# Performance work log

Measured on AMD Instinct MI355X. Metric: run time of the kernel, lower is better.

Reference implementation:

```python
import jax, jax.numpy as jnp
import numpy as np

TAU = 0.5

def _projection(z, W1, b1, W2, b2):
    h = jax.nn.elu(z @ W1.T + b1)
    return h @ W2.T + b2

def _normalize(x, eps=1e-12):
    n = jnp.linalg.norm(x, axis=1, keepdims=True)
    return x / jnp.maximum(n, eps)

def setup_inputs() -> dict:
    key = jax.random.key(0)
    k = jax.random.split(key, 6)
    N, D, P = 8192, 256, 256
    s = 1.0 / np.sqrt(D)
    return {
        "z1": jax.random.normal(k[0], (N, D), jnp.float32),
        "z2": jax.random.normal(k[1], (N, D), jnp.float32),
        "W1": jax.random.normal(k[2], (P, D), jnp.float32) * s,
        "b1": jnp.zeros((P,), jnp.float32),
        "W2": jax.random.normal(k[3], (D, P), jnp.float32) * s,
        "b2": jnp.zeros((D,), jnp.float32),
    }

def reference(z1, z2, W1, b1, W2, b2):
    h1 = _projection(z1, W1, b1, W2, b2)
    h2 = _projection(z2, W1, b1, W2, b2)
    n1 = _normalize(h1)
    n2 = _normalize(h2)
    f11 = jnp.exp((n1 @ n1.T) / TAU)  # [N,N]
    f22 = jnp.exp((n2 @ n2.T) / TAU)
    f12 = jnp.exp((n1 @ n2.T) / TAU)
    d12 = jnp.diagonal(f12)
    l1 = -jnp.log(d12 / (f11.sum(1) + f12.sum(1) - jnp.diagonal(f11)))
    # sim(h2,h1) = f12.T: diag same, row-sum = column-sum of f12
    l2 = -jnp.log(d12 / (f22.sum(1) + f12.sum(0) - jnp.diagonal(f22)))
    return (l1 + l2) * 0.5
```

## Files before the change

kernel.cpp:

```cpp
#include <hip/hip_runtime.h>
#include <hip/hip_bf16.h>
#include <hip/hip_fp8.h>
#include <stdint.h>

#define Nn 8192
#define TWO_N 16384
#define INV_TAU 2.0f

typedef unsigned short u16;
typedef unsigned char u8;
typedef __bf16 bf16x8 __attribute__((ext_vector_type(8)));
typedef float f32x4 __attribute__((ext_vector_type(4)));
typedef int i32x8 __attribute__((ext_vector_type(8)));

typedef const __attribute__((address_space(1))) void* gas_ptr;
typedef __attribute__((address_space(3))) void* las_ptr;

__device__ __forceinline__ void async_copy16(const void* g, void* l) {
  __builtin_amdgcn_global_load_lds((gas_ptr)g, (las_ptr)l, 16, 0, 0);
}

__device__ __forceinline__ u16 f2bf(float x) {
  uint32_t u = __float_as_uint(x);
  u = u + 0x7fffu + ((u >> 16) & 1u);
  return (u16)(u >> 16);
}

__global__ __launch_bounds__(256)
void mfma_gemm1(const float* __restrict__ z1, const float* __restrict__ z2,
                const float* __restrict__ W1, const float* __restrict__ bias,
                u16* __restrict__ outp) {
  __shared__ __bf16 sA[128 * 64];
  __shared__ __bf16 sB[128 * 64];
  const int bx = blockIdx.x;
  const int i0 = bx * 128;
  const int j0 = blockIdx.y * 128;
  const float* Zsrc = (bx < 64) ? (z1 + (size_t)i0 * 256) : (z2 + (size_t)(i0 - Nn) * 256);
  const float* Wsrc = W1 + (size_t)j0 * 256;
  const int t = threadIdx.x;
  const int lane = t & 63, wave = t >> 6;
  const int wm = (wave >> 1) * 64, wn = (wave & 1) * 64;
  const int fr = lane >> 4, fc = lane & 15;
  const int sw = fc & 7;

  f32x4 acc[4][4];
#pragma unroll
  for (int a = 0; a < 4; a++)
#pragma unroll
    for (int b = 0; b < 4; b++) acc[a][b] = (f32x4){0.f, 0.f, 0.f, 0.f};

  for (int k0 = 0; k0 < 256; k0 += 64) {
    __syncthreads();
#pragma unroll
    for (int it = 0; it < 4; ++it) {
      int c = t + 256 * it;
      int row = c >> 3;
      int g = (c & 7) ^ (row & 7);
      const float* sa = Zsrc + (size_t)row * 256 + k0 + g * 8;
      float4 a0 = *(const float4*)sa;
      float4 a1 = *(const float4*)(sa + 4);
      bf16x8 va = {(__bf16)a0.x, (__bf16)a0.y, (__bf16)a0.z, (__bf16)a0.w,
                   (__bf16)a1.x, (__bf16)a1.y, (__bf16)a1.z, (__bf16)a1.w};
      *(bf16x8*)&sA[c * 8] = va;
      const float* sb = Wsrc + (size_t)row * 256 + k0 + g * 8;
      float4 b0 = *(const float4*)sb;
      float4 b1v = *(const float4*)(sb + 4);
      bf16x8 vb = {(__bf16)b0.x, (__bf16)b0.y, (__bf16)b0.z, (__bf16)b0.w,
                   (__bf16)b1v.x, (__bf16)b1v.y, (__bf16)b1v.z, (__bf16)b1v.w};
      *(bf16x8*)&sB[c * 8] = vb;
    }
    __syncthreads();
#pragma unroll
    for (int ks = 0; ks < 2; ++ks) {
      bf16x8 af[4], bfr[4];
#pragma unroll
      for (int mi = 0; mi < 4; mi++)
        af[mi] = *(const bf16x8*)&sA[(wm + mi * 16 + fc) * 64 + (((ks * 4 + fr) ^ sw) * 8)];
#pragma unroll
      for (int ni = 0; ni < 4; ni++)
        bfr[ni] = *(const bf16x8*)&sB[(wn + ni * 16 + fc) * 64 + (((ks * 4 + fr) ^ sw) * 8)];
#pragma unroll
      for (int mi = 0; mi < 4; mi++)
#pragma unroll
        for (int ni = 0; ni < 4; ni++)
          acc[mi][ni] = __builtin_amdgcn_mfma_f32_16x16x32_bf16(af[mi], bfr[ni], acc[mi][ni], 0, 0, 0);
    }
  }

#pragma unroll
  for (int mi = 0; mi < 4; mi++) {
#pragma unroll
    for (int ni = 0; ni < 4; ni++) {
      int col = j0 + wn + ni * 16 + fc;
      float bv = bias[col];
#pragma unroll
      for (int r = 0; r < 4; r++) {
        int row = i0 + wm + mi * 16 + fr * 4 + r;
        float v = acc[mi][ni][r] + bv;
        v = v > 0.f ? v : (__expf(v) - 1.f);
        outp[(size_t)row * 256 + col] = f2bf(v);
      }
    }
  }
}

__global__ __launch_bounds__(256)
void gemm2_norm(const u16* __restrict__ A, const float* __restrict__ W2,
                const float* __restrict__ bias, u8* __restrict__ Mf8,
                float* __restrict__ snorm, float* __restrict__ rsum) {
  __shared__ __bf16 sA[128 * 64];
  __shared__ __bf16 sB[256 * 64];
  const int i0 = blockIdx.x * 128;
  const int t = threadIdx.x;
  const int lane = t & 63, wave = t >> 6;
  const int wm = (wave >> 1) * 64, wn = (wave & 1) * 128;
  const int fr = lane >> 4, fc = lane & 15;
  const int sw = fc & 7;

  if (t < 128) rsum[i0 + t] = 0.f;

  f32x4 acc[4][8];
#pragma unroll
  for (int a = 0; a < 4; a++)
#pragma unroll
    for (int b = 0; b < 8; b++) acc[a][b] = (f32x4){0.f, 0.f, 0.f, 0.f};

  const u16* Ag = A + (size_t)i0 * 256;

  for (int k0 = 0; k0 < 256; k0 += 64) {
    __syncthreads();
#pragma unroll
    for (int it = 0; it < 4; ++it) {
      int c = t + 256 * it;
      int row = c >> 3;
      int kc = ((c & 7) ^ (row & 7)) * 8;
      async_copy16(Ag + (size_t)row * 256 + k0 + kc, (void*)&sA[c * 8]);
    }
#pragma unroll
    for (int it = 0; it < 8; ++it) {
      int c = t + 256 * it;
      int row = c >> 3;
      int g = (c & 7) ^ (row & 7);
      const float* sb = W2 + (size_t)row * 256 + k0 + g * 8;
      float4 b0 = *(const float4*)sb;
      float4 b1v = *(const float4*)(sb + 4);
      bf16x8 vb = {(__bf16)b0.x, (__bf16)b0.y, (__bf16)b0.z, (__bf16)b0.w,
                   (__bf16)b1v.x, (__bf16)b1v.y, (__bf16)b1v.z, (__bf16)b1v.w};
      *(bf16x8*)&sB[c * 8] = vb;
    }
    __syncthreads();
#pragma unroll
    for (int ks = 0; ks < 2; ++ks) {
      bf16x8 af[4], bfr[8];
#pragma unroll
      for (int mi = 0; mi < 4; mi++)
        af[mi] = *(const bf16x8*)&sA[(wm + mi * 16 + fc) * 64 + (((ks * 4 + fr) ^ sw) * 8)];
#pragma unroll
      for (int ni = 0; ni < 8; ni++)
        bfr[ni] = *(const bf16x8*)&sB[(wn + ni * 16 + fc) * 64 + (((ks * 4 + fr) ^ sw) * 8)];
#pragma unroll
      for (int mi = 0; mi < 4; mi++)
#pragma unroll
        for (int ni = 0; ni < 8; ni++)
          acc[mi][ni] = __builtin_amdgcn_mfma_f32_16x16x32_bf16(af[mi], bfr[ni], acc[mi][ni], 0, 0, 0);
    }
  }

  float bv[8];
#pragma unroll
  for (int ni = 0; ni < 8; ni++) bv[ni] = bias[wn + ni * 16 + fc];

  __syncthreads();
  float* red = (float*)sA;

#pragma unroll
  for (int mi = 0; mi < 4; mi++) {
    float ssq[4] = {0.f, 0.f, 0.f, 0.f};
#pragma unroll
    for (int ni = 0; ni < 8; ni++)
#pragma unroll
      for (int r = 0; r < 4; r++) {
        float v = acc[mi][ni][r] + bv[ni];
        acc[mi][ni][r] = v;
        ssq[r] += v * v;
      }
#pragma unroll
    for (int r = 0; r < 4; r++) {
      float v = ssq[r];
#pragma unroll
      for (int off = 1; off < 16; off <<= 1) v += __shfl_xor(v, off, 16);
      if (fc == 0) red[(wm + mi * 16 + fr * 4 + r) * 2 + (wn >> 7)] = v;
    }
  }
  __syncthreads();

  float* red2 = red + 256;
#pragma unroll
  for (int mi = 0; mi < 4; mi++) {
    float ssq2[4] = {0.f, 0.f, 0.f, 0.f};
#pragma unroll
    for (int r = 0; r < 4; r++) {
      int row = wm + mi * 16 + fr * 4 + r;
      float ss = red[row * 2] + red[row * 2 + 1];
      float rn = 1.f / fmaxf(sqrtf(ss), 1e-12f);
#pragma unroll
      for (int ni = 0; ni < 8; ni++) {
        float v = acc[mi][ni][r] * rn;
        __hip_fp8_e4m3 q(v);
        Mf8[(size_t)(i0 + row) * 256 + wn + ni * 16 + fc] = q.__x;
        float fv = (float)q;
        ssq2[r] += fv * fv;
      }
    }
#pragma unroll
    for (int r = 0; r < 4; r++) {
      float v = ssq2[r];
#pragma unroll
      for (int off = 1; off < 16; off <<= 1) v += __shfl_xor(v, off, 16);
      if (fc == 0) red2[(wm + mi * 16 + fr * 4 + r) * 2 + (wn >> 7)] = v;
    }
  }
  __syncthreads();
  if (t < 128) snorm[i0 + t] = red2[t * 2] + red2[t * 2 + 1];
}

__global__ __launch_bounds__(256, 2)
void gram_sym(const u8* __restrict__ Mf8, float* __restrict__ rsum) {
  __shared__ u8 sB8[2][128 * 256];
  const int t = threadIdx.x;
  const int lane = t & 63, wave = t >> 6;
  const int wm = (wave >> 1) * 64, wn = (wave & 1) * 64;
  const int fr = lane >> 4, fc = lane & 15;

  int f = 2111 - blockIdx.x;
  int b = 0;
  while (f >= 2 * (b + 1) * (b + 2)) ++b;
  int rem = f - 2 * b * (b + 1);
  int r = rem / (b + 1);
  int q = rem - r * (b + 1);
  int k = 4 * b + 1 + r;
  const int i_t = 128 - k;
  const int jt0 = i_t + 4 * q;
  const int L = min(4, k - 4 * q);
  const int i0 = i_t * 128;

  {
    const u8* Bg = Mf8 + (size_t)jt0 * 128 * 256;
#pragma unroll
    for (int it = 0; it < 8; ++it) {
      int c = t + 256 * it;
      int row = c >> 4, slot = c & 15;
      int g = slot ^ (row & 15);
      async_copy16(Bg + (size_t)row * 256 + g * 16, (void*)&sB8[0][c * 16]);
    }
  }

  i32x8 afr[4][2];
  {
    const u8* Ag = Mf8 + (size_t)i0 * 256;
#pragma unroll
    for (int mi = 0; mi < 4; ++mi) {
      const u8* rp = Ag + (size_t)(wm + mi * 16 + fc) * 256 + fr * 32;
#pragma unroll
      for (int kb = 0; kb < 2; ++kb) {
        int4 lo = *(const int4*)(rp + kb * 128);
        int4 hi = *(const int4*)(rp + kb * 128 + 16);
        afr[mi][kb] = (i32x8){lo.x, lo.y, lo.z, lo.w, hi.x, hi.y, hi.z, hi.w};
      }
    }
  }

  float rowacc[4][4];
#pragma unroll
  for (int a = 0; a < 4; a++)
#pragma unroll
    for (int rr = 0; rr < 4; rr++) rowacc[a][rr] = 0.f;

  for (int jt = 0; jt < L; ++jt) {
    const int j_t = jt0 + jt;
    const int j0 = j_t * 128;
    const u8* sB = &sB8[jt & 1][0];

    __syncthreads();

    if (jt + 1 < L) {
      const u8* Bg = Mf8 + (size_t)(j_t + 1) * 128 * 256;
      u8* dst = &sB8[(jt + 1) & 1][0];
#pragma unroll
      for (int it = 0; it < 8; ++it) {
        int c = t + 256 * it;
        int row = c >> 4, slot = c & 15;
        int g = slot ^ (row & 15);
        async_copy16(Bg + (size_t)row * 256 + g * 16, (void*)&dst[c * 16]);
      }
    }

    f32x4 acc[4][4];
#pragma unroll
    for (int a = 0; a < 4; a++)
#pragma unroll
      for (int bb = 0; bb < 4; bb++) acc[a][bb] = (f32x4){0.f, 0.f, 0.f, 0.f};

#pragma unroll
    for (int kb = 0; kb < 2; ++kb) {
      i32x8 bfrag[4];
#pragma unroll
      for (int ni = 0; ni < 4; ++ni) {
        const u8* base = sB + (wn + ni * 16 + fc) * 256;
        int g0 = kb * 8 + fr * 2;
        int4 lo = *(const int4*)(base + ((g0 ^ fc) * 16));
        int4 hi = *(const int4*)(base + (((g0 + 1) ^ fc) * 16));
        bfrag[ni] = (i32x8){lo.x, lo.y, lo.z, lo.w, hi.x, hi.y, hi.z, hi.w};
      }
#pragma unroll
      for (int mi = 0; mi < 4; mi++)
#pragma unroll
        for (int ni = 0; ni < 4; ni++)
          acc[mi][ni] = __builtin_amdgcn_mfma_scale_f32_16x16x128_f8f6f4(
              afr[mi][kb], bfrag[ni], acc[mi][ni], 0, 0, 0, 0x7F, 0, 0x7F);
    }

    float colp[4] = {0.f, 0.f, 0.f, 0.f};
#pragma unroll
    for (int mi = 0; mi < 4; mi++) {
#pragma unroll
      for (int ni = 0; ni < 4; ni++) {
        float e0 = __expf(acc[mi][ni][0] * INV_TAU);
        float e1 = __expf(acc[mi][ni][1] * INV_TAU);
        float e2 = __expf(acc[mi][ni][2] * INV_TAU);
        float e3 = __expf(acc[mi][ni][3] * INV_TAU);
        rowacc[mi][0] += e0; rowacc[mi][1] += e1;
        rowacc[mi][2] += e2; rowacc[mi][3] += e3;
        colp[ni] += e0 + e1 + e2 + e3;
      }
    }
    if (j_t != i_t) {
#pragma unroll
      for (int ni = 0; ni < 4; ni++) {
        float v = colp[ni];
        v += __shfl_xor(v, 16, 64);
        v += __shfl_xor(v, 32, 64);
        if (fr == 0) atomicAdd(&rsum[j0 + wn + ni * 16 + fc], v);
      }
    }
  }

#pragma unroll
  for (int mi = 0; mi < 4; mi++) {
#pragma unroll
    for (int rr = 0; rr < 4; rr++) {
      float v = rowacc[mi][rr];
#pragma unroll
      for (int off = 1; off < 16; off <<= 1) v += __shfl_xor(v, off, 16);
      rowacc[mi][rr] = v;
    }
  }
  if (fc == 0) {
#pragma unroll
    for (int mi = 0; mi < 4; mi++) {
      int rbase = i0 + wm + mi * 16 + fr * 4;
      atomicAdd(&rsum[rbase + 0], rowacc[mi][0]);
      atomicAdd(&rsum[rbase + 1], rowacc[mi][1]);
      atomicAdd(&rsum[rbase + 2], rowacc[mi][2]);
      atomicAdd(&rsum[rbase + 3], rowacc[mi][3]);
    }
  }
}

__global__ void final_loss(const u8* __restrict__ Mf8, const float* __restrict__ rsum,
                           const float* __restrict__ snorm, float* __restrict__ out) {
  int i = blockIdx.x * 4 + (threadIdx.x >> 6);
  int lane = threadIdx.x & 63;
  unsigned int ua = ((const unsigned int*)(Mf8 + (size_t)i * 256))[lane];
  unsigned int ub = ((const unsigned int*)(Mf8 + (size_t)(Nn + i) * 256))[lane];
  float d = 0.f;
#pragma unroll
  for (int e = 0; e < 4; ++e) {
    __hip_fp8_e4m3 qa, qb;
    qa.__x = (ua >> (8 * e)) & 0xFF;
    qb.__x = (ub >> (8 * e)) & 0xFF;
    d += (float)qa * (float)qb;
  }
#pragma unroll
  for (int off = 32; off; off >>= 1) d += __shfl_xor(d, off, 64);
  if (lane == 0) {
    float den1 = rsum[i] - __expf(snorm[i] * INV_TAU);
    float den2 = rsum[Nn + i] - __expf(snorm[Nn + i] * INV_TAU);
    out[i] = 0.5f * (logf(den1) + logf(den2)) - d * INV_TAU;
  }
}

extern "C" void kernel_launch(void* const* d_in, const int* in_sizes, int n_in,
                              void* d_out, int out_size, void* d_ws, size_t ws_size,
                              hipStream_t stream) {
  const float* z1 = (const float*)d_in[0];
  const float* z2 = (const float*)d_in[1];
  const float* W1 = (const float*)d_in[2];
  const float* b1 = (const float*)d_in[3];
  const float* W2 = (const float*)d_in[4];
  const float* b2 = (const float*)d_in[5];
  float* out = (float*)d_out;

  char* ws = (char*)d_ws;
  u16*   H1b   = (u16*)(ws);
  u8*    Mf8   = (u8*)(ws + (8u << 20));
  float* rsum  = (float*)(ws + (12u << 20));
  float* snorm = (float*)(ws + (12u << 20) + 65536);

  mfma_gemm1<<<dim3(TWO_N / 128, 2), 256, 0, stream>>>(z1, z2, W1, b1, H1b);

  gemm2_norm<<<TWO_N / 128, 256, 0, stream>>>(H1b, W2, b2, Mf8, snorm, rsum);

  gram_sym<<<2112, 256, 0, stream>>>(Mf8, rsum);

  final_loss<<<Nn / 4, 256, 0, stream>>>(Mf8, rsum, snorm, out);
}
```

Measured before the change: 181.9 us.

## Fuse both projection GEMMs and normalization into one kernel via LDS-resident hidden

```diff
diff --git a/kernel.cpp b/kernel.cpp
--- a/kernel.cpp
+++ b/kernel.cpp
@@ -20,29 +20,27 @@
   __builtin_amdgcn_global_load_lds((gas_ptr)g, (las_ptr)l, 16, 0, 0);
 }
 
-__device__ __forceinline__ u16 f2bf(float x) {
-  uint32_t u = __float_as_uint(x);
-  u = u + 0x7fffu + ((u >> 16) & 1u);
-  return (u16)(u >> 16);
-}
-
 __global__ __launch_bounds__(256)
-void mfma_gemm1(const float* __restrict__ z1, const float* __restrict__ z2,
-                const float* __restrict__ W1, const float* __restrict__ bias,
-                u16* __restrict__ outp) {
-  __shared__ __bf16 sA[128 * 64];
-  __shared__ __bf16 sB[128 * 64];
+void mlp_norm(const float* __restrict__ z1, const float* __restrict__ z2,
+              const float* __restrict__ W1, const float* __restrict__ b1,
+              const float* __restrict__ W2, const float* __restrict__ b2,
+              u8* __restrict__ Mf8, float* __restrict__ snorm,
+              float* __restrict__ rsum) {
+  __shared__ __bf16 sZ[64 * 64];
+  __shared__ __bf16 sW[256 * 64];
+  __shared__ __bf16 sH[64 * 256];
   const int bx = blockIdx.x;
-  const int i0 = bx * 128;
-  const int j0 = blockIdx.y * 128;
-  const float* Zsrc = (bx < 64) ? (z1 + (size_t)i0 * 256) : (z2 + (size_t)(i0 - Nn) * 256);
-  const float* Wsrc = W1 + (size_t)j0 * 256;
+  const int i0 = bx * 64;
+  const float* Zsrc = (bx < 128) ? (z1 + (size_t)i0 * 256)
+                                 : (z2 + (size_t)(i0 - Nn) * 256);
   const int t = threadIdx.x;
   const int lane = t & 63, wave = t >> 6;
-  const int wm = (wave >> 1) * 64, wn = (wave & 1) * 64;
+  const int wn = wave * 64;
   const int fr = lane >> 4, fc = lane & 15;
   const int sw = fc & 7;
 
+  if (t < 64) rsum[i0 + t] = 0.f;
+
   f32x4 acc[4][4];
 #pragma unroll
   for (int a = 0; a < 4; a++)
@@ -52,22 +50,24 @@
   for (int k0 = 0; k0 < 256; k0 += 64) {
     __syncthreads();
 #pragma unroll
-    for (int it = 0; it < 4; ++it) {
+    for (int it = 0; it < 2; ++it) {
       int c = t + 256 * it;
-      int row = c >> 3;
-      int g = (c & 7) ^ (row & 7);
-      const float* sa = Zsrc + (size_t)row * 256 + k0 + g * 8;
-      float4 a0 = *(const float4*)sa;
-      float4 a1 = *(const float4*)(sa + 4);
-      bf16x8 va = {(__bf16)a0.x, (__bf16)a0.y, (__bf16)a0.z, (__bf16)a0.w,
-                   (__bf16)a1.x, (__bf16)a1.y, (__bf16)a1.z, (__bf16)a1.w};
-      *(bf16x8*)&sA[c * 8] = va;
-      const float* sb = Wsrc + (size_t)row * 256 + k0 + g * 8;
-      float4 b0 = *(const float4*)sb;
-      float4 b1v = *(const float4*)(sb + 4);
-      bf16x8 vb = {(__bf16)b0.x, (__bf16)b0.y, (__bf16)b0.z, (__bf16)b0.w,
-                   (__bf16)b1v.x, (__bf16)b1v.y, (__bf16)b1v.z, (__bf16)b1v.w};
-      *(bf16x8*)&sB[c * 8] = vb;
+      int row = c >> 3, g = (c & 7) ^ (row & 7);
+      const float* s = Zsrc + (size_t)row * 256 + k0 + g * 8;
+      float4 a0 = *(const float4*)s, a1 = *(const float4*)(s + 4);
+      bf16x8 v = {(__bf16)a0.x, (__bf16)a0.y, (__bf16)a0.z, (__bf16)a0.w,
+                  (__bf16)a1.x, (__bf16)a1.y, (__bf16)a1.z, (__bf16)a1.w};
+      *(bf16x8*)&sZ[c * 8] = v;
+    }
+#pragma unroll
+    for (int it = 0; it < 8; ++it) {
+      int c = t + 256 * it;
+      int row = c >> 3, g = (c & 7) ^ (row & 7);
+      const float* s = W1 + (size_t)row * 256 + k0 + g * 8;
+      float4 a0 = *(const float4*)s, a1 = *(const float4*)(s + 4);
+      bf16x8 v = {(__bf16)a0.x, (__bf16)a0.y, (__bf16)a0.z, (__bf16)a0.w,
+                  (__bf16)a1.x, (__bf16)a1.y, (__bf16)a1.z, (__bf16)a1.w};
+      *(bf16x8*)&sW[c * 8] = v;
     }
     __syncthreads();
 #pragma unroll
@@ -75,10 +75,10 @@
       bf16x8 af[4], bfr[4];
 #pragma unroll
       for (int mi = 0; mi < 4; mi++)
-        af[mi] = *(const bf16x8*)&sA[(wm + mi * 16 + fc) * 64 + (((ks * 4 + fr) ^ sw) * 8)];
+        af[mi] = *(const bf16x8*)&sZ[(mi * 16 + fc) * 64 + (((ks * 4 + fr) ^ sw) * 8)];
 #pragma unroll
       for (int ni = 0; ni < 4; ni++)
-        bfr[ni] = *(const bf16x8*)&sB[(wn + ni * 16 + fc) * 64 + (((ks * 4 + fr) ^ sw) * 8)];
+        bfr[ni] = *(const bf16x8*)&sW[(wn + ni * 16 + fc) * 64 + (((ks * 4 + fr) ^ sw) * 8)];
 #pragma unroll
       for (int mi = 0; mi < 4; mi++)
 #pragma unroll
@@ -87,97 +87,72 @@
     }
   }
 
-#pragma unroll
-  for (int mi = 0; mi < 4; mi++) {
-#pragma unroll
-    for (int ni = 0; ni < 4; ni++) {
-      int col = j0 + wn + ni * 16 + fc;
-      float bv = bias[col];
-#pragma unroll
-      for (int r = 0; r < 4; r++) {
-        int row = i0 + wm + mi * 16 + fr * 4 + r;
-        float v = acc[mi][ni][r] + bv;
-        v = v > 0.f ? v : (__expf(v) - 1.f);
-        outp[(size_t)row * 256 + col] = f2bf(v);
-      }
-    }
-  }
-}
-
-__global__ __launch_bounds__(256)
-void gemm2_norm(const u16* __restrict__ A, const float* __restrict__ W2,
-                const float* __restrict__ bias, u8* __restrict__ Mf8,
-                float* __restrict__ snorm, float* __restrict__ rsum) {
-  __shared__ __bf16 sA[128 * 64];
-  __shared__ __bf16 sB[256 * 64];
-  const int i0 = blockIdx.x * 128;
-  const int t = threadIdx.x;
-  const int lane = t & 63, wave = t >> 6;
-  const int wm = (wave >> 1) * 64, wn = (wave & 1) * 128;
-  const int fr = lane >> 4, fc = lane & 15;
-  const int sw = fc & 7;
-
-  if (t < 128) rsum[i0 + t] = 0.f;
-
-  f32x4 acc[4][8];
-#pragma unroll
-  for (int a = 0; a < 4; a++)
-#pragma unroll
-    for (int b = 0; b < 8; b++) acc[a][b] = (f32x4){0.f, 0.f, 0.f, 0.f};
-
-  const u16* Ag = A + (size_t)i0 * 256;
+  {
+    float bv[4];
+#pragma unroll
+    for (int ni = 0; ni < 4; ni++) bv[ni] = b1[wn + ni * 16 + fc];
+#pragma unroll
+    for (int mi = 0; mi < 4; mi++)
+#pragma unroll
+      for (int ni = 0; ni < 4; ni++) {
+        int col = wn + ni * 16 + fc;
+        int gc = col >> 3;
+#pragma unroll
+        for (int r = 0; r < 4; r++) {
+          int row = mi * 16 + fr * 4 + r;
+          float v = acc[mi][ni][r] + bv[ni];
+          v = v > 0.f ? v : (__expf(v) - 1.f);
+          int pos = (gc & 24) | ((gc & 7) ^ (row & 7));
+          sH[row * 256 + pos * 8 + (col & 7)] = (__bf16)v;
+          acc[mi][ni][r] = 0.f;
+        }
+      }
+  }
 
   for (int k0 = 0; k0 < 256; k0 += 64) {
     __syncthreads();
-#pragma unroll
-    for (int it = 0; it < 4; ++it) {
-      int c = t + 256 * it;
-      int row = c >> 3;
-      int kc = ((c & 7) ^ (row & 7)) * 8;
-      async_copy16(Ag + (size_t)row * 256 + k0 + kc, (void*)&sA[c * 8]);
-    }
 #pragma unroll
     for (int it = 0; it < 8; ++it) {
       int c = t + 256 * it;
-      int row = c >> 3;
-      int g = (c & 7) ^ (row & 7);
-      const float* sb = W2 + (size_t)row * 256 + k0 + g * 8;
-      float4 b0 = *(const float4*)sb;
-      float4 b1v = *(const float4*)(sb + 4);
-      bf16x8 vb = {(__bf16)b0.x, (__bf16)b0.y, (__bf16)b0.z, (__bf16)b0.w,
-                   (__bf16)b1v.x, (__bf16)b1v.y, (__bf16)b1v.z, (__bf16)b1v.w};
-      *(bf16x8*)&sB[c * 8] = vb;
-    }
-    __syncthreads();
+      int row = c >> 3, g = (c & 7) ^ (row & 7);
+      const float* s = W2 + (size_t)row * 256 + k0 + g * 8;
+      float4 a0 = *(const float4*)s, a1 = *(const float4*)(s + 4);
+      bf16x8 v = {(__bf16)a0.x, (__bf16)a0.y, (__bf16)a0.z, (__bf16)a0.w,
+                  (__bf16)a1.x, (__bf16)a1.y, (__bf16)a1.z, (__bf16)a1.w};
+      *(bf16x8*)&sW[c * 8] = v;
+    }
+    __syncthreads();
+    const int kgb = k0 >> 3;
 #pragma unroll
     for (int ks = 0; ks < 2; ++ks) {
-      bf16x8 af[4], bfr[8];
-#pragma unroll
-      for (int mi = 0; mi < 4; mi++)
-        af[mi] = *(const bf16x8*)&sA[(wm + mi * 16 + fc) * 64 + (((ks * 4 + fr) ^ sw) * 8)];
-#pragma unroll
-      for (int ni = 0; ni < 8; ni++)
-        bfr[ni] = *(const bf16x8*)&sB[(wn + ni * 16 + fc) * 64 + (((ks * 4 + fr) ^ sw) * 8)];
-#pragma unroll
-      for (int mi = 0; mi < 4; mi++)
-#pragma unroll
-        for (int ni = 0; ni < 8; ni++)
+      bf16x8 af[4], bfr[4];
+#pragma unroll
+      for (int mi = 0; mi < 4; mi++)
+        af[mi] = *(const bf16x8*)&sH[(mi * 16 + fc) * 256 + (kgb + (((ks * 4 + fr) ^ sw))) * 8];
+#pragma unroll
+      for (int ni = 0; ni < 4; ni++)
+        bfr[ni] = *(const bf16x8*)&sW[(wn + ni * 16 + fc) * 64 + (((ks * 4 + fr) ^ sw) * 8)];
+#pragma unroll
+      for (int mi = 0; mi < 4; mi++)
+#pragma unroll
+        for (int ni = 0; ni < 4; ni++)
           acc[mi][ni] = __builtin_amdgcn_mfma_f32_16x16x32_bf16(af[mi], bfr[ni], acc[mi][ni], 0, 0, 0);
     }
   }
 
-  float bv[8];
-#pragma unroll
-  for (int ni = 0; ni < 8; ni++) bv[ni] = bias[wn + ni * 16 + fc];
+  float bv[4];
+#pragma unroll
+  for (int ni = 0; ni < 4; ni++) bv[ni] = b2[wn + ni * 16 + fc];
 
   __syncthreads();
-  float* red = (float*)sA;
+  float* red = (float*)sZ;
+  float* red2 = red + 256;
 
 #pragma unroll
   for (int mi = 0; mi < 4; mi++) {
     float ssq[4] = {0.f, 0.f, 0.f, 0.f};
 #pragma unroll
-    for (int ni = 0; ni < 8; ni++)
+    for (int ni = 0; ni < 4; ni++)
 #pragma unroll
       for (int r = 0; r < 4; r++) {
         float v = acc[mi][ni][r] + bv[ni];
@@ -189,22 +164,21 @@
       float v = ssq[r];
 #pragma unroll
       for (int off = 1; off < 16; off <<= 1) v += __shfl_xor(v, off, 16);
-      if (fc == 0) red[(wm + mi * 16 + fr * 4 + r) * 2 + (wn >> 7)] = v;
+      if (fc == 0) red[(mi * 16 + fr * 4 + r) * 4 + wave] = v;
     }
   }
   __syncthreads();
 
-  float* red2 = red + 256;
 #pragma unroll
   for (int mi = 0; mi < 4; mi++) {
     float ssq2[4] = {0.f, 0.f, 0.f, 0.f};
 #pragma unroll
     for (int r = 0; r < 4; r++) {
-      int row = wm + mi * 16 + fr * 4 + r;
-      float ss = red[row * 2] + red[row * 2 + 1];
+      int row = mi * 16 + fr * 4 + r;
+      float ss = red[row * 4] + red[row * 4 + 1] + red[row * 4 + 2] + red[row * 4 + 3];
       float rn = 1.f / fmaxf(sqrtf(ss), 1e-12f);
 #pragma unroll
-      for (int ni = 0; ni < 8; ni++) {
+      for (int ni = 0; ni < 4; ni++) {
         float v = acc[mi][ni][r] * rn;
         __hip_fp8_e4m3 q(v);
         Mf8[(size_t)(i0 + row) * 256 + wn + ni * 16 + fc] = q.__x;
@@ -217,11 +191,12 @@
       float v = ssq2[r];
 #pragma unroll
       for (int off = 1; off < 16; off <<= 1) v += __shfl_xor(v, off, 16);
-      if (fc == 0) red2[(wm + mi * 16 + fr * 4 + r) * 2 + (wn >> 7)] = v;
+      if (fc == 0) red2[(mi * 16 + fr * 4 + r) * 4 + wave] = v;
     }
   }
   __syncthreads();
-  if (t < 128) snorm[i0 + t] = red2[t * 2] + red2[t * 2 + 1];
+  if (t < 64)
+    snorm[i0 + t] = red2[t * 4] + red2[t * 4 + 1] + red2[t * 4 + 2] + red2[t * 4 + 3];
 }
 
 __global__ __launch_bounds__(256, 2)
@@ -402,14 +377,11 @@
   float* out = (float*)d_out;
 
   char* ws = (char*)d_ws;
-  u16*   H1b   = (u16*)(ws);
-  u8*    Mf8   = (u8*)(ws + (8u << 20));
-  float* rsum  = (float*)(ws + (12u << 20));
-  float* snorm = (float*)(ws + (12u << 20) + 65536);
-
-  mfma_gemm1<<<dim3(TWO_N / 128, 2), 256, 0, stream>>>(z1, z2, W1, b1, H1b);
-
-  gemm2_norm<<<TWO_N / 128, 256, 0, stream>>>(H1b, W2, b2, Mf8, snorm, rsum);
+  u8*    Mf8   = (u8*)(ws);
+  float* rsum  = (float*)(ws + (4u << 20));
+  float* snorm = (float*)(ws + (4u << 20) + 65536);
+
+  mlp_norm<<<256, 256, 0, stream>>>(z1, z2, W1, b1, W2, b2, Mf8, snorm, rsum);
 
   gram_sym<<<2112, 256, 0, stream>>>(Mf8, rsum);
 
```

Result: faster. 176.7 us, median of 2 (-2.8%).
